# Kernel optimization log

Hardware: AMD Instinct MI355X
Metric: run time of the kernel (lower is better)

The kernel has to match this reference:

```python
import jax, jax.numpy as jnp
import numpy as np

GAMMA = 20
LAMBDA_INV = 25.0


def setup_inputs() -> dict:
    key = jax.random.key(0)
    k1, k2 = jax.random.split(key)
    B, P, D = 128, 512, 384
    z = jax.random.normal(k1, (B, P, D), dtype=jnp.float32)
    view_ids = jax.random.randint(k2, (P,), 0, 2, dtype=jnp.int64)
    return {"z": z, "view_ids": view_ids}


def reference(z, view_ids):
    B, P, D = z.shape
    # [B, P, P] pairwise similarity per image
    sim = jnp.einsum('bpd,bqd->bpq', z, z)
    # valid pairs: different view and not self
    mask_view = view_ids[None, :] != view_ids[:, None]          # [P, P]
    mask = mask_view & ~jnp.eye(P, dtype=bool)
    sim = jnp.where(mask[None, :, :], sim, jnp.float32(-1.0))
    best_sim = sim.max(axis=2)                                   # [B, P]
    best_j = sim.argmax(axis=2)                                  # [B, P]
    # flatten across batch, global top-gamma anchors
    best_sim_flat = best_sim.reshape(-1)                         # [B*P]
    offsets = jnp.arange(B, dtype=best_j.dtype)[:, None] * P
    best_j_flat = (best_j + offsets).reshape(-1)                 # [B*P]
    topk_vals, topk_idx = jax.lax.top_k(best_sim_flat, GAMMA)
    z_flat = z.reshape(-1, D)
    z1 = z_flat[topk_idx]                                        # anchors
    z2 = z_flat[best_j_flat[topk_idx]]                           # matches
    loss = LAMBDA_INV * jnp.mean((z1 - z2) ** 2)
    fmatch_avg_cos = jax.lax.stop_gradient(topk_vals.mean())
    return loss, fmatch_avg_cos
```

## Files before the change

### kernel.cpp

```cpp
#include <hip/hip_runtime.h>


#define NB 128
#define NP 512
#define ND 384
#define NGAMMA 20
#define NKS 12

typedef __attribute__((ext_vector_type(8))) short short8;
typedef __attribute__((ext_vector_type(4))) float f32x4;

__device__ __forceinline__ unsigned short f2bf(float f) {
    unsigned int u = __float_as_uint(f);
    u += 0x7fffu + ((u >> 16) & 1u);
    return (unsigned short)(u >> 16);
}

__device__ __forceinline__ void gload16(const void* gptr, void* lptr) {
    __builtin_amdgcn_global_load_lds(
        (const __attribute__((address_space(1))) void*)gptr,
        (__attribute__((address_space(3))) void*)lptr, 16, 0, 0);
}

__global__ __launch_bounds__(256) void fm_convert(
    const float* __restrict__ z, unsigned short* __restrict__ zt)
{
    __shared__ float ls[128][36];

    const int tid  = threadIdx.x;
    const int bid  = blockIdx.x;
    const int b    = bid / (NKS * 4);
    const int rem  = bid % (NKS * 4);
    const int kt   = rem >> 2;
    const int pblk = rem & 3;

    const float* zsrc = z + ((size_t)b * NP + pblk * 128) * ND + kt * 32;
#pragma unroll
    for (int i = 0; i < 4; ++i) {
        const int f   = tid + i * 256;
        const int row = f >> 3, c4 = f & 7;
        const float4 v = *(const float4*)(zsrc + (size_t)row * ND + c4 * 4);
        *(float4*)&ls[row][c4 * 4] = v;
    }
    __syncthreads();

    const int kg = tid >> 6, lane = tid & 63;
    unsigned short* dst = zt + (((size_t)b * NKS + kt) * 4 + kg) * 4096
                             + (size_t)pblk * 128 * 8;
#pragma unroll
    for (int it = 0; it < 2; ++it) {
        const int row = it * 64 + lane;
        const float4 v0 = *(const float4*)&ls[row][kg * 8];
        const float4 v1 = *(const float4*)&ls[row][kg * 8 + 4];
        short8 s;
        s[0] = (short)f2bf(v0.x); s[1] = (short)f2bf(v0.y);
        s[2] = (short)f2bf(v0.z); s[3] = (short)f2bf(v0.w);
        s[4] = (short)f2bf(v1.x); s[5] = (short)f2bf(v1.y);
        s[6] = (short)f2bf(v1.z); s[7] = (short)f2bf(v1.w);
        *(short8*)(dst + (size_t)row * 8) = s;
    }
}

__global__ __launch_bounds__(256, 3) void fm_gemm(
    const unsigned short* __restrict__ zt, const int* __restrict__ view,
    float* __restrict__ pval, int* __restrict__ pidx)
{
    __shared__ __align__(16) unsigned short Ah[3][4][128][8];
    __shared__ __align__(16) unsigned short Bh[3][4][128][8];
    __shared__ int vs[NP];
    float* lsv = (float*)&Ah[0][0][0][0];
    int*   lsi = (int*)lsv + 256;
    float* lqv = (float*)((int*)lsv + 512);
    int*   lqi = (int*)lsv + 768;

    const int tid  = threadIdx.x;
    const int lane = tid & 63;
    const int wid  = tid >> 6;
    const int wr   = wid >> 1, wc = wid & 1;
    const int g    = lane >> 4, r = lane & 15;

    const int bid  = blockIdx.x;
    const int gidx = (bid & 7) * 160 + (bid >> 3);
    const int b    = gidx / 10;
    const int t    = gidx % 10;
    int tr, tc;
    if (t < 4)      { tr = 0; tc = t; }
    else if (t < 7) { tr = 1; tc = t - 3; }
    else if (t < 9) { tr = 2; tc = t - 5; }
    else            { tr = 3; tc = 3; }
    const bool diag = (tr == tc);
    const int p0 = tr * 128, q0 = tc * 128;

    vs[tid]       = view[tid];
    vs[tid + 256] = view[tid + 256];
    __builtin_amdgcn_sched_barrier(0);

    f32x4 acc[4][4];
#pragma unroll
    for (int mi = 0; mi < 4; ++mi)
#pragma unroll
        for (int ni = 0; ni < 4; ++ni) acc[mi][ni] = (f32x4){0.f, 0.f, 0.f, 0.f};

#define STAGE(BUF, KT)                                                           \
    do {                                                                         \
        _Pragma("unroll")                                                        \
        for (int i = 0; i < 2; ++i) {                                            \
            const int c_  = wid * 2 + i;                                         \
            const int kg_ = c_ >> 1;                                             \
            const int rb_ = (c_ & 1) * 64;                                       \
            const size_t pl_ = (((size_t)b * NKS + (KT)) * 4 + kg_) * 4096;      \
            gload16(zt + pl_ + (size_t)(p0 + rb_ + lane) * 8,                    \
                    &Ah[BUF][kg_][rb_][0]);                                      \
            gload16(zt + pl_ + (size_t)(q0 + rb_ + lane) * 8,                    \
                    &Bh[BUF][kg_][rb_][0]);                                      \
        }                                                                        \
    } while (0)

#define COMPUTE(BUF)                                                             \
    do {                                                                         \
        short8 ah_[4], bh_[4];                                                   \
        _Pragma("unroll")                                                        \
        for (int mi = 0; mi < 4; ++mi)                                           \
            ah_[mi] = *(const short8*)&Ah[BUF][g][wr * 64 + mi * 16 + r][0];     \
        _Pragma("unroll")                                                        \
        for (int ni = 0; ni < 4; ++ni)                                           \
            bh_[ni] = *(const short8*)&Bh[BUF][g][wc * 64 + ni * 16 + r][0];     \
        _Pragma("unroll")                                                        \
        for (int mi = 0; mi < 4; ++mi)                                           \
            _Pragma("unroll")                                                    \
            for (int ni = 0; ni < 4; ++ni)                                       \
                acc[mi][ni] = __builtin_amdgcn_mfma_f32_16x16x32_bf16(           \
                    ah_[mi], bh_[ni], acc[mi][ni], 0, 0, 0);                     \
    } while (0)

    STAGE(0, 0);
    STAGE(1, 1);
#pragma unroll
    for (int kt = 0; kt < NKS; ++kt) {
        if (kt < NKS - 1) asm volatile("s_waitcnt vmcnt(4)" ::: "memory");
        else              asm volatile("s_waitcnt vmcnt(0)" ::: "memory");
        __builtin_amdgcn_s_barrier();
        __builtin_amdgcn_sched_barrier(0);
        if (kt + 2 < NKS) STAGE((kt + 2) % 3, kt + 2);
        __builtin_amdgcn_sched_barrier(0);
        COMPUTE(kt % 3);
    }
#undef STAGE
#undef COMPUTE

#pragma unroll
    for (int mi = 0; mi < 4; ++mi) {
#pragma unroll
        for (int j = 0; j < 4; ++j) {
            const int prow = p0 + wr * 64 + mi * 16 + g * 4 + j;
            const int rv = vs[prow];
            float bv = -2.0f; int bq = 0;
#pragma unroll
            for (int ni = 0; ni < 4; ++ni) {
                const int q = q0 + wc * 64 + ni * 16 + r;
                const float v = (vs[q] != rv) ? acc[mi][ni][j] : -1.0f;
                if (v > bv) { bv = v; bq = q; }
            }
#pragma unroll
            for (int off = 1; off < 16; off <<= 1) {
                const float ov = __shfl_xor(bv, off);
                const int   oq = __shfl_xor(bq, off);
                if (ov > bv || (ov == bv && oq < bq)) { bv = ov; bq = oq; }
            }
            if (r == 0) {
                lsv[(wr * 2 + wc) * 64 + mi * 16 + g * 4 + j] = bv;
                lsi[(wr * 2 + wc) * 64 + mi * 16 + g * 4 + j] = bq;
            }
        }
    }
    if (!diag) {
#pragma unroll
        for (int ni = 0; ni < 4; ++ni) {
            const int q = q0 + wc * 64 + ni * 16 + r;
            const int qv = vs[q];
            float bv = -2.0f; int bp = 0;
#pragma unroll
            for (int mi = 0; mi < 4; ++mi)
#pragma unroll
                for (int j = 0; j < 4; ++j) {
                    const int prow = p0 + wr * 64 + mi * 16 + g * 4 + j;
                    const float v = (vs[prow] != qv) ? acc[mi][ni][j] : -1.0f;
                    if (v > bv) { bv = v; bp = prow; }
                }
#pragma unroll
            for (int off = 16; off < 64; off <<= 1) {
                const float ov = __shfl_xor(bv, off);
                const int   op = __shfl_xor(bp, off);
                if (ov > bv || (ov == bv && op < bp)) { bv = ov; bp = op; }
            }
            if (g == 0) {
                lqv[(wc * 2 + wr) * 64 + ni * 16 + r] = bv;
                lqi[(wc * 2 + wr) * 64 + ni * 16 + r] = bp;
            }
        }
    }
    __syncthreads();
    if (tid < 128) {
        const int half = tid >> 6, row = tid & 63;
        {
            float v0 = lsv[(half * 2 + 0) * 64 + row]; int i0 = lsi[(half * 2 + 0) * 64 + row];
            const float v1 = lsv[(half * 2 + 1) * 64 + row]; const int i1 = lsi[(half * 2 + 1) * 64 + row];
            if (v1 > v0) { v0 = v1; i0 = i1; }
            const int p = p0 + half * 64 + row;
            pval[((size_t)b * NP + p) * 4 + tc] = v0;
            pidx[((size_t)b * NP + p) * 4 + tc] = i0;
        }
        if (!diag) {
            float v0 = lqv[(half * 2 + 0) * 64 + row]; int i0 = lqi[(half * 2 + 0) * 64 + row];
            const float v1 = lqv[(half * 2 + 1) * 64 + row]; const int i1 = lqi[(half * 2 + 1) * 64 + row];
            if (v1 > v0) { v0 = v1; i0 = i1; }
            const int q = q0 + half * 64 + row;
            pval[((size_t)b * NP + q) * 4 + tr] = v0;
            pidx[((size_t)b * NP + q) * 4 + tr] = i0;
        }
    }
}

__global__ __launch_bounds__(64) void fm_topk_local(
    const float* __restrict__ pval, float* __restrict__ cval, int* __restrict__ cidx)
{
    const int lane = threadIdx.x;
    const int base = blockIdx.x * 1024;
    float v[16]; int id[16];
#pragma unroll
    for (int i = 0; i < 16; ++i) {
        const int a = base + i * 64 + lane;
        const float4 pv = ((const float4*)pval)[a];
        float bv = pv.x;
        if (pv.y > bv) bv = pv.y;
        if (pv.z > bv) bv = pv.z;
        if (pv.w > bv) bv = pv.w;
        v[i] = bv; id[i] = a;
    }
    for (int it = 0; it < NGAMMA; ++it) {
        float bv = v[0]; int bi = id[0];
#pragma unroll
        for (int i = 1; i < 16; ++i)
            if (v[i] > bv || (v[i] == bv && id[i] < bi)) { bv = v[i]; bi = id[i]; }
#pragma unroll
        for (int off = 1; off < 64; off <<= 1) {
            const float ov = __shfl_xor(bv, off);
            const int   oi = __shfl_xor(bi, off);
            if (ov > bv || (ov == bv && oi < bi)) { bv = ov; bi = oi; }
        }
        if (lane == 0) {
            cval[blockIdx.x * NGAMMA + it] = bv;
            cidx[blockIdx.x * NGAMMA + it] = bi;
        }
#pragma unroll
        for (int i = 0; i < 16; ++i) if (id[i] == bi) v[i] = -1e30f;
    }
}

__global__ __launch_bounds__(256) void fm_final(
    const float* __restrict__ cval, const int* __restrict__ cidx,
    const float* __restrict__ pval, const int* __restrict__ pidx,
    const float* __restrict__ z, float* __restrict__ out)
{
    __shared__ int sel[NGAMMA];
    __shared__ int selj[NGAMMA];
    __shared__ float red[4];

    const int t = threadIdx.x;
    const int lane = t & 63, w = t >> 6;
    float ssum = 0.f;

    if (w == 0) {
        float v[20]; int id[20];
#pragma unroll
        for (int i = 0; i < 20; ++i) {
            const int e = i * 64 + lane;
            v[i] = cval[e]; id[i] = cidx[e];
        }
        for (int it = 0; it < NGAMMA; ++it) {
            float bv = v[0]; int bi = id[0];
#pragma unroll
            for (int i = 1; i < 20; ++i)
                if (v[i] > bv || (v[i] == bv && id[i] < bi)) { bv = v[i]; bi = id[i]; }
#pragma unroll
            for (int off = 1; off < 64; off <<= 1) {
                const float ov = __shfl_xor(bv, off);
                const int   oi = __shfl_xor(bi, off);
                if (ov > bv || (ov == bv && oi < bi)) { bv = ov; bi = oi; }
            }
            if (lane == 0) sel[it] = bi;
            ssum += bv;
#pragma unroll
            for (int i = 0; i < 20; ++i) if (id[i] == bi) v[i] = -1e30f;
        }
        if (lane < NGAMMA) {
            const int a = sel[lane];
            const float4 pv = ((const float4*)pval)[a];
            float bv = pv.x; int bc = 0;
            if (pv.y > bv) { bv = pv.y; bc = 1; }
            if (pv.z > bv) { bv = pv.z; bc = 2; }
            if (pv.w > bv) { bv = pv.w; bc = 3; }
            selj[lane] = ((a >> 9) << 9) + pidx[(size_t)a * 4 + bc];
        }
    }
    __syncthreads();

    float acc = 0.f;
    for (int pr = 0; pr < NGAMMA; ++pr) {
        const int a = sel[pr];
        const int j = selj[pr];
        const float* za = z + (size_t)a * ND;
        const float* zj = z + (size_t)j * ND;
        for (int d = t; d < ND; d += 256) {
            const float df = za[d] - zj[d];
            acc = fmaf(df, df, acc);
        }
    }
#pragma unroll
    for (int off = 1; off < 64; off <<= 1) acc += __shfl_xor(acc, off);
    if (lane == 0) red[w] = acc;
    __syncthreads();
    if (t == 0) {
        const float tot = red[0] + red[1] + red[2] + red[3];
        out[0] = 25.0f * tot / (float)(NGAMMA * ND);
        out[1] = ssum / (float)NGAMMA;
    }
}

extern "C" void kernel_launch(void* const* d_in, const int* in_sizes, int n_in,
                              void* d_out, int out_size, void* d_ws, size_t ws_size,
                              hipStream_t stream)
{
    const float* z    = (const float*)d_in[0];
    const int*   view = (const int*)d_in[1];
    float*       out  = (float*)d_out;
    char* ws = (char*)d_ws;

    const size_t zt_off   = 0;
    const size_t pval_off = (size_t)NB * NP * ND * 2;
    const size_t pidx_off = pval_off + (size_t)NB * NP * 4 * 4;
    const size_t cval_off = pidx_off + (size_t)NB * NP * 4 * 4;
    const size_t cidx_off = cval_off + 64 * NGAMMA * 4;

    unsigned short* zt = (unsigned short*)(ws + zt_off);
    float* pval = (float*)(ws + pval_off);
    int*   pidx = (int*)(ws + pidx_off);
    float* cval = (float*)(ws + cval_off);
    int*   cidx = (int*)(ws + cidx_off);

    fm_convert<<<NB * NKS * 4, 256, 0, stream>>>(z, zt);
    fm_gemm<<<NB * 10, 256, 0, stream>>>(zt, view, pval, pidx);
    fm_topk_local<<<(NB * NP) / 1024, 64, 0, stream>>>(pval, cval, cidx);
    fm_final<<<1, 256, 0, stream>>>(cval, cidx, pval, pidx, z, out);
}
```

Measured before the change: 134.5 us.

## Fuse all four stages into one persistent kernel with grid barriers

Replaces the four separate launches (convert, gemm, local top-k, final) with a single persistent kernel of 512 blocks that loops over the conversion tasks and GEMM tiles, separated by atomic-counter grid barriers. The local top-k is reworked to use 256 threads per block, and the final reduction waits on a counter. This is meant to remove launch gaps and tail effects between kernels. In exchange it adds spin-wait barriers, drops GEMM occupancy from 3 to 2 blocks per CU, and relies on all 512 blocks being co-resident, which can deadlock if they are not.

```diff
diff --git a/kernel.cpp b/kernel.cpp
--- a/kernel.cpp
+++ b/kernel.cpp
@@ -6,6 +6,8 @@
 #define ND 384
 #define NGAMMA 20
 #define NKS 12
+#define GRID 512
+#define NTILE 1280
 
 typedef __attribute__((ext_vector_type(8))) short short8;
 typedef __attribute__((ext_vector_type(4))) float f32x4;
@@ -22,96 +24,91 @@
         (__attribute__((address_space(3))) void*)lptr, 16, 0, 0);
 }
 
-__global__ __launch_bounds__(256) void fm_convert(
-    const float* __restrict__ z, unsigned short* __restrict__ zt)
+__device__ __forceinline__ void grid_sync(int* cnt, int target) {
+    __syncthreads();
+    if (threadIdx.x == 0) {
+        __threadfence();
+        __hip_atomic_fetch_add(cnt, 1, __ATOMIC_RELEASE, __HIP_MEMORY_SCOPE_AGENT);
+        while (__hip_atomic_load(cnt, __ATOMIC_RELAXED, __HIP_MEMORY_SCOPE_AGENT) < target)
+            __builtin_amdgcn_s_sleep(2);
+        __threadfence();
+    }
+    __syncthreads();
+}
+
+__global__ __launch_bounds__(256, 2) void fm_fused(
+    const float* __restrict__ z, const int* __restrict__ view,
+    unsigned short* __restrict__ zt,
+    float* __restrict__ pval, int* __restrict__ pidx,
+    float* __restrict__ cval, int* __restrict__ cidx,
+    int* __restrict__ cnt, float* __restrict__ out)
 {
-    __shared__ float ls[128][36];
+    __shared__ __align__(16) char lds[51200];
+    unsigned short (*Ah)[4][128][8] = (unsigned short(*)[4][128][8])lds;
+    unsigned short (*Bh)[4][128][8] = (unsigned short(*)[4][128][8])(lds + 24576);
+    int* vs = (int*)(lds + 49152);
 
     const int tid  = threadIdx.x;
     const int bid  = blockIdx.x;
-    const int b    = bid / (NKS * 4);
-    const int rem  = bid % (NKS * 4);
-    const int kt   = rem >> 2;
-    const int pblk = rem & 3;
-
-    const float* zsrc = z + ((size_t)b * NP + pblk * 128) * ND + kt * 32;
-#pragma unroll
-    for (int i = 0; i < 4; ++i) {
-        const int f   = tid + i * 256;
-        const int row = f >> 3, c4 = f & 7;
-        const float4 v = *(const float4*)(zsrc + (size_t)row * ND + c4 * 4);
-        *(float4*)&ls[row][c4 * 4] = v;
-    }
-    __syncthreads();
-
-    const int kg = tid >> 6, lane = tid & 63;
-    unsigned short* dst = zt + (((size_t)b * NKS + kt) * 4 + kg) * 4096
-                             + (size_t)pblk * 128 * 8;
-#pragma unroll
-    for (int it = 0; it < 2; ++it) {
-        const int row = it * 64 + lane;
-        const float4 v0 = *(const float4*)&ls[row][kg * 8];
-        const float4 v1 = *(const float4*)&ls[row][kg * 8 + 4];
-        short8 s;
-        s[0] = (short)f2bf(v0.x); s[1] = (short)f2bf(v0.y);
-        s[2] = (short)f2bf(v0.z); s[3] = (short)f2bf(v0.w);
-        s[4] = (short)f2bf(v1.x); s[5] = (short)f2bf(v1.y);
-        s[6] = (short)f2bf(v1.z); s[7] = (short)f2bf(v1.w);
-        *(short8*)(dst + (size_t)row * 8) = s;
-    }
-}
-
-__global__ __launch_bounds__(256, 3) void fm_gemm(
-    const unsigned short* __restrict__ zt, const int* __restrict__ view,
-    float* __restrict__ pval, int* __restrict__ pidx)
-{
-    __shared__ __align__(16) unsigned short Ah[3][4][128][8];
-    __shared__ __align__(16) unsigned short Bh[3][4][128][8];
-    __shared__ int vs[NP];
-    float* lsv = (float*)&Ah[0][0][0][0];
-    int*   lsi = (int*)lsv + 256;
-    float* lqv = (float*)((int*)lsv + 512);
-    int*   lqi = (int*)lsv + 768;
-
-    const int tid  = threadIdx.x;
     const int lane = tid & 63;
     const int wid  = tid >> 6;
     const int wr   = wid >> 1, wc = wid & 1;
     const int g    = lane >> 4, r = lane & 15;
 
-    const int bid  = blockIdx.x;
-    const int gidx = (bid & 7) * 160 + (bid >> 3);
-    const int b    = gidx / 10;
-    const int t    = gidx % 10;
-    int tr, tc;
-    if (t < 4)      { tr = 0; tc = t; }
-    else if (t < 7) { tr = 1; tc = t - 3; }
-    else if (t < 9) { tr = 2; tc = t - 5; }
-    else            { tr = 3; tc = 3; }
-    const bool diag = (tr == tc);
-    const int p0 = tr * 128, q0 = tc * 128;
+    {
+        float (*ls)[36] = (float(*)[36])lds;
+        for (int i = 0; i < 12; ++i) {
+            const int task = bid * 12 + i;
+            const int b    = task / (NKS * 4);
+            const int rem  = task % (NKS * 4);
+            const int kt   = rem >> 2;
+            const int pblk = rem & 3;
+            const float* zsrc = z + ((size_t)b * NP + pblk * 128) * ND + kt * 32;
+#pragma unroll
+            for (int k = 0; k < 4; ++k) {
+                const int f = tid + k * 256, row = f >> 3, c4 = f & 7;
+                *(float4*)&ls[row][c4 * 4] =
+                    *(const float4*)(zsrc + (size_t)row * ND + c4 * 4);
+            }
+            __syncthreads();
+            const int kg = wid;
+            unsigned short* dst = zt + (((size_t)b * NKS + kt) * 4 + kg) * 4096
+                                     + (size_t)pblk * 1024;
+#pragma unroll
+            for (int it = 0; it < 2; ++it) {
+                const int row = it * 64 + lane;
+                const float4 v0 = *(const float4*)&ls[row][kg * 8];
+                const float4 v1 = *(const float4*)&ls[row][kg * 8 + 4];
+                short8 s;
+                s[0] = (short)f2bf(v0.x); s[1] = (short)f2bf(v0.y);
+                s[2] = (short)f2bf(v0.z); s[3] = (short)f2bf(v0.w);
+                s[4] = (short)f2bf(v1.x); s[5] = (short)f2bf(v1.y);
+                s[6] = (short)f2bf(v1.z); s[7] = (short)f2bf(v1.w);
+                *(short8*)(dst + (size_t)row * 8) = s;
+            }
+            __syncthreads();
+        }
+    }
+    grid_sync(cnt + 0, GRID);
 
     vs[tid]       = view[tid];
     vs[tid + 256] = view[tid + 256];
-    __builtin_amdgcn_sched_barrier(0);
-
-    f32x4 acc[4][4];
-#pragma unroll
-    for (int mi = 0; mi < 4; ++mi)
-#pragma unroll
-        for (int ni = 0; ni < 4; ++ni) acc[mi][ni] = (f32x4){0.f, 0.f, 0.f, 0.f};
-
-#define STAGE(BUF, KT)                                                           \
+    float* lsv = (float*)lds;
+    int*   lsi = (int*)lds + 256;
+    float* lqv = (float*)lds + 512;
+    int*   lqi = (int*)lds + 768;
+
+#define STAGE(BUF, KT, P0, Q0, BB)                                               \
     do {                                                                         \
         _Pragma("unroll")                                                        \
-        for (int i = 0; i < 2; ++i) {                                            \
-            const int c_  = wid * 2 + i;                                         \
+        for (int i_ = 0; i_ < 2; ++i_) {                                         \
+            const int c_  = wid * 2 + i_;                                        \
             const int kg_ = c_ >> 1;                                             \
             const int rb_ = (c_ & 1) * 64;                                       \
-            const size_t pl_ = (((size_t)b * NKS + (KT)) * 4 + kg_) * 4096;      \
-            gload16(zt + pl_ + (size_t)(p0 + rb_ + lane) * 8,                    \
+            const size_t pl_ = (((size_t)(BB) * NKS + (KT)) * 4 + kg_) * 4096;   \
+            gload16(zt + pl_ + (size_t)((P0) + rb_ + lane) * 8,                  \
                     &Ah[BUF][kg_][rb_][0]);                                      \
-            gload16(zt + pl_ + (size_t)(q0 + rb_ + lane) * 8,                    \
+            gload16(zt + pl_ + (size_t)((Q0) + rb_ + lane) * 8,                  \
                     &Bh[BUF][kg_][rb_][0]);                                      \
         }                                                                        \
     } while (0)
@@ -133,144 +130,182 @@
                     ah_[mi], bh_[ni], acc[mi][ni], 0, 0, 0);                     \
     } while (0)
 
-    STAGE(0, 0);
-    STAGE(1, 1);
-#pragma unroll
-    for (int kt = 0; kt < NKS; ++kt) {
-        if (kt < NKS - 1) asm volatile("s_waitcnt vmcnt(4)" ::: "memory");
-        else              asm volatile("s_waitcnt vmcnt(0)" ::: "memory");
-        __builtin_amdgcn_s_barrier();
-        __builtin_amdgcn_sched_barrier(0);
-        if (kt + 2 < NKS) STAGE((kt + 2) % 3, kt + 2);
-        __builtin_amdgcn_sched_barrier(0);
-        COMPUTE(kt % 3);
+    for (int pass = 0; pass < 3; ++pass) {
+        const int x = bid + pass * 512;
+        if (x >= NTILE) break;
+        const int gidx = (x & 7) * 160 + (x >> 3);
+        const int b    = gidx / 10;
+        const int t    = gidx % 10;
+        int tr, tc;
+        if (t < 4)      { tr = 0; tc = t; }
+        else if (t < 7) { tr = 1; tc = t - 3; }
+        else if (t < 9) { tr = 2; tc = t - 5; }
+        else            { tr = 3; tc = 3; }
+        const bool diag = (tr == tc);
+        const int p0 = tr * 128, q0 = tc * 128;
+
+        f32x4 acc[4][4];
+#pragma unroll
+        for (int mi = 0; mi < 4; ++mi)
+#pragma unroll
+            for (int ni = 0; ni < 4; ++ni) acc[mi][ni] = (f32x4){0.f, 0.f, 0.f, 0.f};
+
+        __syncthreads();
+        STAGE(0, 0, p0, q0, b);
+        STAGE(1, 1, p0, q0, b);
+#pragma unroll
+        for (int kt = 0; kt < NKS; ++kt) {
+            if (kt < NKS - 1) asm volatile("s_waitcnt vmcnt(4)" ::: "memory");
+            else              asm volatile("s_waitcnt vmcnt(0)" ::: "memory");
+            __builtin_amdgcn_s_barrier();
+            __builtin_amdgcn_sched_barrier(0);
+            if (kt + 2 < NKS) STAGE((kt + 2) % 3, kt + 2, p0, q0, b);
+            __builtin_amdgcn_sched_barrier(0);
+            COMPUTE(kt % 3);
+        }
+
+#pragma unroll
+        for (int mi = 0; mi < 4; ++mi) {
+#pragma unroll
+            for (int j = 0; j < 4; ++j) {
+                const int prow = p0 + wr * 64 + mi * 16 + g * 4 + j;
+                const int rv = vs[prow];
+                float bv = -2.0f; int bq = 0;
+#pragma unroll
+                for (int ni = 0; ni < 4; ++ni) {
+                    const int q = q0 + wc * 64 + ni * 16 + r;
+                    const float v = (vs[q] != rv) ? acc[mi][ni][j] : -1.0f;
+                    if (v > bv) { bv = v; bq = q; }
+                }
+#pragma unroll
+                for (int off = 1; off < 16; off <<= 1) {
+                    const float ov = __shfl_xor(bv, off);
+                    const int   oq = __shfl_xor(bq, off);
+                    if (ov > bv || (ov == bv && oq < bq)) { bv = ov; bq = oq; }
+                }
+                if (r == 0) {
+                    lsv[(wr * 2 + wc) * 64 + mi * 16 + g * 4 + j] = bv;
+                    lsi[(wr * 2 + wc) * 64 + mi * 16 + g * 4 + j] = bq;
+                }
+            }
+        }
+        if (!diag) {
+#pragma unroll
+            for (int ni = 0; ni < 4; ++ni) {
+                const int q = q0 + wc * 64 + ni * 16 + r;
+                const int qv = vs[q];
+                float bv = -2.0f; int bp = 0;
+#pragma unroll
+                for (int mi = 0; mi < 4; ++mi)
+#pragma unroll
+                    for (int j = 0; j < 4; ++j) {
+                        const int prow = p0 + wr * 64 + mi * 16 + g * 4 + j;
+                        const float v = (vs[prow] != qv) ? acc[mi][ni][j] : -1.0f;
+                        if (v > bv) { bv = v; bp = prow; }
+                    }
+#pragma unroll
+                for (int off = 16; off < 64; off <<= 1) {
+                    const float ov = __shfl_xor(bv, off);
+                    const int   op = __shfl_xor(bp, off);
+                    if (ov > bv || (ov == bv && op < bp)) { bv = ov; bp = op; }
+                }
+                if (g == 0) {
+                    lqv[(wc * 2 + wr) * 64 + ni * 16 + r] = bv;
+                    lqi[(wc * 2 + wr) * 64 + ni * 16 + r] = bp;
+                }
+            }
+        }
+        __syncthreads();
+        if (tid < 128) {
+            const int half = tid >> 6, row = tid & 63;
+            {
+                float v0 = lsv[(half * 2 + 0) * 64 + row]; int i0 = lsi[(half * 2 + 0) * 64 + row];
+                const float v1 = lsv[(half * 2 + 1) * 64 + row]; const int i1 = lsi[(half * 2 + 1) * 64 + row];
+                if (v1 > v0) { v0 = v1; i0 = i1; }
+                const int p = p0 + half * 64 + row;
+                pval[((size_t)b * NP + p) * 4 + tc] = v0;
+                pidx[((size_t)b * NP + p) * 4 + tc] = i0;
+            }
+            if (!diag) {
+                float v0 = lqv[(half * 2 + 0) * 64 + row]; int i0 = lqi[(half * 2 + 0) * 64 + row];
+                const float v1 = lqv[(half * 2 + 1) * 64 + row]; const int i1 = lqi[(half * 2 + 1) * 64 + row];
+                if (v1 > v0) { v0 = v1; i0 = i1; }
+                const int q = q0 + half * 64 + row;
+                pval[((size_t)b * NP + q) * 4 + tr] = v0;
+                pidx[((size_t)b * NP + q) * 4 + tr] = i0;
+            }
+        }
     }
 #undef STAGE
 #undef COMPUTE
-
-#pragma unroll
-    for (int mi = 0; mi < 4; ++mi) {
-#pragma unroll
-        for (int j = 0; j < 4; ++j) {
-            const int prow = p0 + wr * 64 + mi * 16 + g * 4 + j;
-            const int rv = vs[prow];
-            float bv = -2.0f; int bq = 0;
-#pragma unroll
-            for (int ni = 0; ni < 4; ++ni) {
-                const int q = q0 + wc * 64 + ni * 16 + r;
-                const float v = (vs[q] != rv) ? acc[mi][ni][j] : -1.0f;
-                if (v > bv) { bv = v; bq = q; }
-            }
-#pragma unroll
-            for (int off = 1; off < 16; off <<= 1) {
-                const float ov = __shfl_xor(bv, off);
-                const int   oq = __shfl_xor(bq, off);
-                if (ov > bv || (ov == bv && oq < bq)) { bv = ov; bq = oq; }
-            }
-            if (r == 0) {
-                lsv[(wr * 2 + wc) * 64 + mi * 16 + g * 4 + j] = bv;
-                lsi[(wr * 2 + wc) * 64 + mi * 16 + g * 4 + j] = bq;
-            }
-        }
-    }
-    if (!diag) {
-#pragma unroll
-        for (int ni = 0; ni < 4; ++ni) {
-            const int q = q0 + wc * 64 + ni * 16 + r;
-            const int qv = vs[q];
-            float bv = -2.0f; int bp = 0;
-#pragma unroll
-            for (int mi = 0; mi < 4; ++mi)
-#pragma unroll
-                for (int j = 0; j < 4; ++j) {
-                    const int prow = p0 + wr * 64 + mi * 16 + g * 4 + j;
-                    const float v = (vs[prow] != qv) ? acc[mi][ni][j] : -1.0f;
-                    if (v > bv) { bv = v; bp = prow; }
-                }
-#pragma unroll
-            for (int off = 16; off < 64; off <<= 1) {
-                const float ov = __shfl_xor(bv, off);
-                const int   op = __shfl_xor(bp, off);
-                if (ov > bv || (ov == bv && op < bp)) { bv = ov; bp = op; }
-            }
-            if (g == 0) {
-                lqv[(wc * 2 + wr) * 64 + ni * 16 + r] = bv;
-                lqi[(wc * 2 + wr) * 64 + ni * 16 + r] = bp;
-            }
-        }
-    }
-    __syncthreads();
-    if (tid < 128) {
-        const int half = tid >> 6, row = tid & 63;
-        {
-            float v0 = lsv[(half * 2 + 0) * 64 + row]; int i0 = lsi[(half * 2 + 0) * 64 + row];
-            const float v1 = lsv[(half * 2 + 1) * 64 + row]; const int i1 = lsi[(half * 2 + 1) * 64 + row];
-            if (v1 > v0) { v0 = v1; i0 = i1; }
-            const int p = p0 + half * 64 + row;
-            pval[((size_t)b * NP + p) * 4 + tc] = v0;
-            pidx[((size_t)b * NP + p) * 4 + tc] = i0;
-        }
-        if (!diag) {
-            float v0 = lqv[(half * 2 + 0) * 64 + row]; int i0 = lqi[(half * 2 + 0) * 64 + row];
-            const float v1 = lqv[(half * 2 + 1) * 64 + row]; const int i1 = lqi[(half * 2 + 1) * 64 + row];
-            if (v1 > v0) { v0 = v1; i0 = i1; }
-            const int q = q0 + half * 64 + row;
-            pval[((size_t)b * NP + q) * 4 + tr] = v0;
-            pidx[((size_t)b * NP + q) * 4 + tr] = i0;
-        }
-    }
-}
-
-__global__ __launch_bounds__(64) void fm_topk_local(
-    const float* __restrict__ pval, float* __restrict__ cval, int* __restrict__ cidx)
-{
-    const int lane = threadIdx.x;
-    const int base = blockIdx.x * 1024;
-    float v[16]; int id[16];
-#pragma unroll
-    for (int i = 0; i < 16; ++i) {
-        const int a = base + i * 64 + lane;
-        const float4 pv = ((const float4*)pval)[a];
-        float bv = pv.x;
-        if (pv.y > bv) bv = pv.y;
-        if (pv.z > bv) bv = pv.z;
-        if (pv.w > bv) bv = pv.w;
-        v[i] = bv; id[i] = a;
-    }
-    for (int it = 0; it < NGAMMA; ++it) {
-        float bv = v[0]; int bi = id[0];
-#pragma unroll
-        for (int i = 1; i < 16; ++i)
-            if (v[i] > bv || (v[i] == bv && id[i] < bi)) { bv = v[i]; bi = id[i]; }
-#pragma unroll
-        for (int off = 1; off < 64; off <<= 1) {
-            const float ov = __shfl_xor(bv, off);
-            const int   oi = __shfl_xor(bi, off);
-            if (ov > bv || (ov == bv && oi < bi)) { bv = ov; bi = oi; }
-        }
-        if (lane == 0) {
-            cval[blockIdx.x * NGAMMA + it] = bv;
-            cidx[blockIdx.x * NGAMMA + it] = bi;
-        }
-#pragma unroll
-        for (int i = 0; i < 16; ++i) if (id[i] == bi) v[i] = -1e30f;
-    }
-}
-
-__global__ __launch_bounds__(256) void fm_final(
-    const float* __restrict__ cval, const int* __restrict__ cidx,
-    const float* __restrict__ pval, const int* __restrict__ pidx,
-    const float* __restrict__ z, float* __restrict__ out)
-{
-    __shared__ int sel[NGAMMA];
-    __shared__ int selj[NGAMMA];
-    __shared__ float red[4];
-
-    const int t = threadIdx.x;
-    const int lane = t & 63, w = t >> 6;
+    grid_sync(cnt + 1, GRID);
+
+    if (bid >= 64) return;
+
+    {
+        float* sv = (float*)lds;
+        float* wv = (float*)(lds + 4096);
+        int*   wi = (int*)(lds + 4112);
+        const int base = bid * 1024;
+#pragma unroll
+        for (int i = 0; i < 4; ++i) {
+            const int e = tid + 256 * i;
+            const float4 pv = ((const float4*)pval)[base + e];
+            float bv = pv.x;
+            if (pv.y > bv) bv = pv.y;
+            if (pv.z > bv) bv = pv.z;
+            if (pv.w > bv) bv = pv.w;
+            sv[e] = bv;
+        }
+        __syncthreads();
+        for (int it = 0; it < NGAMMA; ++it) {
+            float v = sv[tid];
+            int pos = tid;
+#pragma unroll
+            for (int i = 1; i < 4; ++i) {
+                const int e = tid + 256 * i;
+                const float x2 = sv[e];
+                if (x2 > v || (x2 == v && e < pos)) { v = x2; pos = e; }
+            }
+#pragma unroll
+            for (int off = 1; off < 64; off <<= 1) {
+                const float ov = __shfl_xor(v, off);
+                const int   op = __shfl_xor(pos, off);
+                if (ov > v || (ov == v && op < pos)) { v = ov; pos = op; }
+            }
+            if (lane == 0) { wv[wid] = v; wi[wid] = pos; }
+            __syncthreads();
+            if (tid == 0) {
+                float bv2 = wv[0]; int bp = wi[0];
+                for (int k = 1; k < 4; ++k)
+                    if (wv[k] > bv2 || (wv[k] == bv2 && wi[k] < bp)) { bv2 = wv[k]; bp = wi[k]; }
+                cval[bid * NGAMMA + it] = bv2;
+                cidx[bid * NGAMMA + it] = base + bp;
+                sv[bp] = -1e30f;
+            }
+            __syncthreads();
+        }
+        __syncthreads();
+        if (tid == 0) {
+            __threadfence();
+            __hip_atomic_fetch_add(cnt + 2, 1, __ATOMIC_RELEASE, __HIP_MEMORY_SCOPE_AGENT);
+        }
+    }
+    if (bid != 0) return;
+
+    if (tid == 0) {
+        while (__hip_atomic_load(cnt + 2, __ATOMIC_RELAXED, __HIP_MEMORY_SCOPE_AGENT) < 64)
+            __builtin_amdgcn_s_sleep(2);
+        __threadfence();
+    }
+    __syncthreads();
+
+    int*   sel  = (int*)(lds + 8192);
+    int*   selj = (int*)(lds + 8192 + 128);
+    float* red  = (float*)(lds + 8192 + 256);
     float ssum = 0.f;
 
-    if (w == 0) {
+    if (wid == 0) {
         float v[20]; int id[20];
 #pragma unroll
         for (int i = 0; i < 20; ++i) {
@@ -305,22 +340,22 @@
     }
     __syncthreads();
 
-    float acc = 0.f;
+    float acc2 = 0.f;
     for (int pr = 0; pr < NGAMMA; ++pr) {
         const int a = sel[pr];
         const int j = selj[pr];
         const float* za = z + (size_t)a * ND;
         const float* zj = z + (size_t)j * ND;
-        for (int d = t; d < ND; d += 256) {
+        for (int d = tid; d < ND; d += 256) {
             const float df = za[d] - zj[d];
-            acc = fmaf(df, df, acc);
-        }
-    }
-#pragma unroll
-    for (int off = 1; off < 64; off <<= 1) acc += __shfl_xor(acc, off);
-    if (lane == 0) red[w] = acc;
-    __syncthreads();
-    if (t == 0) {
+            acc2 = fmaf(df, df, acc2);
+        }
+    }
+#pragma unroll
+    for (int off = 1; off < 64; off <<= 1) acc2 += __shfl_xor(acc2, off);
+    if (lane == 0) red[wid] = acc2;
+    __syncthreads();
+    if (tid == 0) {
         const float tot = red[0] + red[1] + red[2] + red[3];
         out[0] = 25.0f * tot / (float)(NGAMMA * ND);
         out[1] = ssum / (float)NGAMMA;
@@ -341,15 +376,15 @@
     const size_t pidx_off = pval_off + (size_t)NB * NP * 4 * 4;
     const size_t cval_off = pidx_off + (size_t)NB * NP * 4 * 4;
     const size_t cidx_off = cval_off + 64 * NGAMMA * 4;
+    const size_t cnt_off  = cidx_off + 64 * NGAMMA * 4;
 
     unsigned short* zt = (unsigned short*)(ws + zt_off);
     float* pval = (float*)(ws + pval_off);
     int*   pidx = (int*)(ws + pidx_off);
     float* cval = (float*)(ws + cval_off);
     int*   cidx = (int*)(ws + cidx_off);
-
-    fm_convert<<<NB * NKS * 4, 256, 0, stream>>>(z, zt);
-    fm_gemm<<<NB * 10, 256, 0, stream>>>(zt, view, pval, pidx);
-    fm_topk_local<<<(NB * NP) / 1024, 64, 0, stream>>>(pval, cval, cidx);
-    fm_final<<<1, 256, 0, stream>>>(cval, cidx, pval, pidx, z, out);
-}
+    int*   cnt  = (int*)(ws + cnt_off);
+
+    hipMemsetAsync(cnt, 0, 3 * sizeof(int), stream);
+    fm_fused<<<GRID, 256, 0, stream>>>(z, view, zt, pval, pidx, cval, cidx, cnt, out);
+}
```

Result: slower. 270.0 us (+100.7%).

## Load GEMM fragments directly from global memory instead of LDS pipeline

Applied to the files above, without the earlier changes.

Removes the triple-buffered global-to-LDS staging with barriers in the similarity GEMM. Each wave now loads its bf16 MFMA operands straight from the pre-swizzled global layout into registers every k-step. This drops LDS traffic, the per-step workgroup barriers and the LDS allocation, which may allow higher occupancy. In exchange, the two waves that share a tile row or column now read the same data from global/L2 twice, and there is no explicit prefetch to hide load latency.

```diff
diff --git a/kernel.cpp b/kernel.cpp
--- a/kernel.cpp
+++ b/kernel.cpp
@@ -14,12 +14,6 @@
     unsigned int u = __float_as_uint(f);
     u += 0x7fffu + ((u >> 16) & 1u);
     return (unsigned short)(u >> 16);
-}
-
-__device__ __forceinline__ void gload16(const void* gptr, void* lptr) {
-    __builtin_amdgcn_global_load_lds(
-        (const __attribute__((address_space(1))) void*)gptr,
-        (__attribute__((address_space(3))) void*)lptr, 16, 0, 0);
 }
 
 __global__ __launch_bounds__(256) void fm_convert(
@@ -39,14 +33,13 @@
     for (int i = 0; i < 4; ++i) {
         const int f   = tid + i * 256;
         const int row = f >> 3, c4 = f & 7;
-        const float4 v = *(const float4*)(zsrc + (size_t)row * ND + c4 * 4);
-        *(float4*)&ls[row][c4 * 4] = v;
+        *(float4*)&ls[row][c4 * 4] = *(const float4*)(zsrc + (size_t)row * ND + c4 * 4);
     }
     __syncthreads();
 
     const int kg = tid >> 6, lane = tid & 63;
     unsigned short* dst = zt + (((size_t)b * NKS + kt) * 4 + kg) * 4096
-                             + (size_t)pblk * 128 * 8;
+                             + (size_t)pblk * 1024;
 #pragma unroll
     for (int it = 0; it < 2; ++it) {
         const int row = it * 64 + lane;
@@ -65,13 +58,11 @@
     const unsigned short* __restrict__ zt, const int* __restrict__ view,
     float* __restrict__ pval, int* __restrict__ pidx)
 {
-    __shared__ __align__(16) unsigned short Ah[3][4][128][8];
-    __shared__ __align__(16) unsigned short Bh[3][4][128][8];
     __shared__ int vs[NP];
-    float* lsv = (float*)&Ah[0][0][0][0];
-    int*   lsi = (int*)lsv + 256;
-    float* lqv = (float*)((int*)lsv + 512);
-    int*   lqi = (int*)lsv + 768;
+    __shared__ float lsv[2][2][64];
+    __shared__ int   lsi[2][2][64];
+    __shared__ float lqv[2][2][64];
+    __shared__ int   lqi[2][2][64];
 
     const int tid  = threadIdx.x;
     const int lane = tid & 63;
@@ -93,7 +84,13 @@
 
     vs[tid]       = view[tid];
     vs[tid + 256] = view[tid + 256];
-    __builtin_amdgcn_sched_barrier(0);
+    __syncthreads();
+
+    const size_t zbB = (size_t)b * (NKS * 4 * 4096);
+    const unsigned short* __restrict__ Az =
+        zt + zbB + (size_t)g * 4096 + (size_t)(p0 + wr * 64 + r) * 8;
+    const unsigned short* __restrict__ Bz =
+        zt + zbB + (size_t)g * 4096 + (size_t)(q0 + wc * 64 + r) * 8;
 
     f32x4 acc[4][4];
 #pragma unroll
@@ -101,52 +98,22 @@
 #pragma unroll
         for (int ni = 0; ni < 4; ++ni) acc[mi][ni] = (f32x4){0.f, 0.f, 0.f, 0.f};
 
-#define STAGE(BUF, KT)                                                           \
-    do {                                                                         \
-        _Pragma("unroll")                                                        \
-        for (int i = 0; i < 2; ++i) {                                            \
-            const int c_  = wid * 2 + i;                                         \
-            const int kg_ = c_ >> 1;                                             \
-            const int rb_ = (c_ & 1) * 64;                                       \
-            const size_t pl_ = (((size_t)b * NKS + (KT)) * 4 + kg_) * 4096;      \
-            gload16(zt + pl_ + (size_t)(p0 + rb_ + lane) * 8,                    \
-                    &Ah[BUF][kg_][rb_][0]);                                      \
-            gload16(zt + pl_ + (size_t)(q0 + rb_ + lane) * 8,                    \
-                    &Bh[BUF][kg_][rb_][0]);                                      \
-        }                                                                        \
-    } while (0)
-
-#define COMPUTE(BUF)                                                             \
-    do {                                                                         \
-        short8 ah_[4], bh_[4];                                                   \
-        _Pragma("unroll")                                                        \
-        for (int mi = 0; mi < 4; ++mi)                                           \
-            ah_[mi] = *(const short8*)&Ah[BUF][g][wr * 64 + mi * 16 + r][0];     \
-        _Pragma("unroll")                                                        \
-        for (int ni = 0; ni < 4; ++ni)                                           \
-            bh_[ni] = *(const short8*)&Bh[BUF][g][wc * 64 + ni * 16 + r][0];     \
-        _Pragma("unroll")                                                        \
-        for (int mi = 0; mi < 4; ++mi)                                           \
-            _Pragma("unroll")                                                    \
-            for (int ni = 0; ni < 4; ++ni)                                       \
-                acc[mi][ni] = __builtin_amdgcn_mfma_f32_16x16x32_bf16(           \
-                    ah_[mi], bh_[ni], acc[mi][ni], 0, 0, 0);                     \
-    } while (0)
-
-    STAGE(0, 0);
-    STAGE(1, 1);
 #pragma unroll
     for (int kt = 0; kt < NKS; ++kt) {
-        if (kt < NKS - 1) asm volatile("s_waitcnt vmcnt(4)" ::: "memory");
-        else              asm volatile("s_waitcnt vmcnt(0)" ::: "memory");
-        __builtin_amdgcn_s_barrier();
-        __builtin_amdgcn_sched_barrier(0);
-        if (kt + 2 < NKS) STAGE((kt + 2) % 3, kt + 2);
-        __builtin_amdgcn_sched_barrier(0);
-        COMPUTE(kt % 3);
-    }
-#undef STAGE
-#undef COMPUTE
+        short8 ah[4], bh[4];
+#pragma unroll
+        for (int mi = 0; mi < 4; ++mi)
+            ah[mi] = *(const short8*)(Az + (size_t)kt * 16384 + mi * 128);
+#pragma unroll
+        for (int ni = 0; ni < 4; ++ni)
+            bh[ni] = *(const short8*)(Bz + (size_t)kt * 16384 + ni * 128);
+#pragma unroll
+        for (int mi = 0; mi < 4; ++mi)
+#pragma unroll
+            for (int ni = 0; ni < 4; ++ni)
+                acc[mi][ni] = __builtin_amdgcn_mfma_f32_16x16x32_bf16(
+                    ah[mi], bh[ni], acc[mi][ni], 0, 0, 0);
+    }
 
 #pragma unroll
     for (int mi = 0; mi < 4; ++mi) {
@@ -168,8 +135,8 @@
                 if (ov > bv || (ov == bv && oq < bq)) { bv = ov; bq = oq; }
             }
             if (r == 0) {
-                lsv[(wr * 2 + wc) * 64 + mi * 16 + g * 4 + j] = bv;
-                lsi[(wr * 2 + wc) * 64 + mi * 16 + g * 4 + j] = bq;
+                lsv[wr][wc][mi * 16 + g * 4 + j] = bv;
+                lsi[wr][wc][mi * 16 + g * 4 + j] = bq;
             }
         }
     }
@@ -194,8 +161,8 @@
                 if (ov > bv || (ov == bv && op < bp)) { bv = ov; bp = op; }
             }
             if (g == 0) {
-                lqv[(wc * 2 + wr) * 64 + ni * 16 + r] = bv;
-                lqi[(wc * 2 + wr) * 64 + ni * 16 + r] = bp;
+                lqv[wc][wr][ni * 16 + r] = bv;
+                lqi[wc][wr][ni * 16 + r] = bp;
             }
         }
     }
@@ -203,16 +170,16 @@
     if (tid < 128) {
         const int half = tid >> 6, row = tid & 63;
         {
-            float v0 = lsv[(half * 2 + 0) * 64 + row]; int i0 = lsi[(half * 2 + 0) * 64 + row];
-            const float v1 = lsv[(half * 2 + 1) * 64 + row]; const int i1 = lsi[(half * 2 + 1) * 64 + row];
+            float v0 = lsv[half][0][row]; int i0 = lsi[half][0][row];
+            const float v1 = lsv[half][1][row]; const int i1 = lsi[half][1][row];
             if (v1 > v0) { v0 = v1; i0 = i1; }
             const int p = p0 + half * 64 + row;
             pval[((size_t)b * NP + p) * 4 + tc] = v0;
             pidx[((size_t)b * NP + p) * 4 + tc] = i0;
         }
         if (!diag) {
-            float v0 = lqv[(half * 2 + 0) * 64 + row]; int i0 = lqi[(half * 2 + 0) * 64 + row];
-            const float v1 = lqv[(half * 2 + 1) * 64 + row]; const int i1 = lqi[(half * 2 + 1) * 64 + row];
+            float v0 = lqv[half][0][row]; int i0 = lqi[half][0][row];
+            const float v1 = lqv[half][1][row]; const int i1 = lqi[half][1][row];
             if (v1 > v0) { v0 = v1; i0 = i1; }
             const int q = q0 + half * 64 + row;
             pval[((size_t)b * NP + q) * 4 + tr] = v0;
```

Measured after the change: 135.1 us. No clear change (+0.4%).

## Use 8-wave GEMM blocks and fuse top-k stages with atomic ticket

Applied to the files above, without the earlier changes.

The similarity GEMM blocks grow from 4 to 8 waves. Each wave now covers a 64x32 sub-tile, and the staging loads are spread so each wave issues one A and one B load per k-step. The local top-k kernel and the final single-block kernel are merged into one kernel. A last-block-done atomic ticket triggers the global top-gamma selection and loss computation, which removes one launch. This adds a memset launch and atomic/fence overhead, and it halves the accumulator work per wave, which may lower MFMA efficiency per wave.

```diff
diff --git a/kernel.cpp b/kernel.cpp
--- a/kernel.cpp
+++ b/kernel.cpp
@@ -39,14 +39,13 @@
     for (int i = 0; i < 4; ++i) {
         const int f   = tid + i * 256;
         const int row = f >> 3, c4 = f & 7;
-        const float4 v = *(const float4*)(zsrc + (size_t)row * ND + c4 * 4);
-        *(float4*)&ls[row][c4 * 4] = v;
+        *(float4*)&ls[row][c4 * 4] = *(const float4*)(zsrc + (size_t)row * ND + c4 * 4);
     }
     __syncthreads();
 
     const int kg = tid >> 6, lane = tid & 63;
     unsigned short* dst = zt + (((size_t)b * NKS + kt) * 4 + kg) * 4096
-                             + (size_t)pblk * 128 * 8;
+                             + (size_t)pblk * 1024;
 #pragma unroll
     for (int it = 0; it < 2; ++it) {
         const int row = it * 64 + lane;
@@ -61,7 +60,7 @@
     }
 }
 
-__global__ __launch_bounds__(256, 3) void fm_gemm(
+__global__ __launch_bounds__(512, 4) void fm_gemm(
     const unsigned short* __restrict__ zt, const int* __restrict__ view,
     float* __restrict__ pval, int* __restrict__ pidx)
 {
@@ -69,14 +68,15 @@
     __shared__ __align__(16) unsigned short Bh[3][4][128][8];
     __shared__ int vs[NP];
     float* lsv = (float*)&Ah[0][0][0][0];
-    int*   lsi = (int*)lsv + 256;
-    float* lqv = (float*)((int*)lsv + 512);
-    int*   lqi = (int*)lsv + 768;
+    int*   lsi = (int*)lsv + 512;
+    float* lqv = (float*)lsv + 1024;
+    int*   lqi = (int*)lsv + 1280;
 
     const int tid  = threadIdx.x;
     const int lane = tid & 63;
     const int wid  = tid >> 6;
-    const int wr   = wid >> 1, wc = wid & 1;
+    const int wr   = wid >> 2;
+    const int wc2  = wid & 3;
     const int g    = lane >> 4, r = lane & 15;
 
     const int bid  = blockIdx.x;
@@ -91,44 +91,37 @@
     const bool diag = (tr == tc);
     const int p0 = tr * 128, q0 = tc * 128;
 
-    vs[tid]       = view[tid];
-    vs[tid + 256] = view[tid + 256];
+    vs[tid] = view[tid];
     __builtin_amdgcn_sched_barrier(0);
 
-    f32x4 acc[4][4];
+    f32x4 acc[4][2];
 #pragma unroll
     for (int mi = 0; mi < 4; ++mi)
 #pragma unroll
-        for (int ni = 0; ni < 4; ++ni) acc[mi][ni] = (f32x4){0.f, 0.f, 0.f, 0.f};
+        for (int ni = 0; ni < 2; ++ni) acc[mi][ni] = (f32x4){0.f, 0.f, 0.f, 0.f};
 
 #define STAGE(BUF, KT)                                                           \
     do {                                                                         \
-        _Pragma("unroll")                                                        \
-        for (int i = 0; i < 2; ++i) {                                            \
-            const int c_  = wid * 2 + i;                                         \
-            const int kg_ = c_ >> 1;                                             \
-            const int rb_ = (c_ & 1) * 64;                                       \
-            const size_t pl_ = (((size_t)b * NKS + (KT)) * 4 + kg_) * 4096;      \
-            gload16(zt + pl_ + (size_t)(p0 + rb_ + lane) * 8,                    \
-                    &Ah[BUF][kg_][rb_][0]);                                      \
-            gload16(zt + pl_ + (size_t)(q0 + rb_ + lane) * 8,                    \
-                    &Bh[BUF][kg_][rb_][0]);                                      \
-        }                                                                        \
+        const int kg_ = wid >> 1;                                                \
+        const int rb_ = (wid & 1) * 64;                                          \
+        const size_t pl_ = (((size_t)b * NKS + (KT)) * 4 + kg_) * 4096;          \
+        gload16(zt + pl_ + (size_t)(p0 + rb_ + lane) * 8, &Ah[BUF][kg_][rb_][0]); \
+        gload16(zt + pl_ + (size_t)(q0 + rb_ + lane) * 8, &Bh[BUF][kg_][rb_][0]); \
     } while (0)
 
 #define COMPUTE(BUF)                                                             \
     do {                                                                         \
-        short8 ah_[4], bh_[4];                                                   \
+        short8 ah_[4], bh_[2];                                                   \
         _Pragma("unroll")                                                        \
         for (int mi = 0; mi < 4; ++mi)                                           \
             ah_[mi] = *(const short8*)&Ah[BUF][g][wr * 64 + mi * 16 + r][0];     \
         _Pragma("unroll")                                                        \
-        for (int ni = 0; ni < 4; ++ni)                                           \
-            bh_[ni] = *(const short8*)&Bh[BUF][g][wc * 64 + ni * 16 + r][0];     \
+        for (int ni = 0; ni < 2; ++ni)                                           \
+            bh_[ni] = *(const short8*)&Bh[BUF][g][wc2 * 32 + ni * 16 + r][0];    \
         _Pragma("unroll")                                                        \
         for (int mi = 0; mi < 4; ++mi)                                           \
             _Pragma("unroll")                                                    \
-            for (int ni = 0; ni < 4; ++ni)                                       \
+            for (int ni = 0; ni < 2; ++ni)                                       \
                 acc[mi][ni] = __builtin_amdgcn_mfma_f32_16x16x32_bf16(           \
                     ah_[mi], bh_[ni], acc[mi][ni], 0, 0, 0);                     \
     } while (0)
@@ -137,7 +130,7 @@
     STAGE(1, 1);
 #pragma unroll
     for (int kt = 0; kt < NKS; ++kt) {
-        if (kt < NKS - 1) asm volatile("s_waitcnt vmcnt(4)" ::: "memory");
+        if (kt < NKS - 1) asm volatile("s_waitcnt vmcnt(2)" ::: "memory");
         else              asm volatile("s_waitcnt vmcnt(0)" ::: "memory");
         __builtin_amdgcn_s_barrier();
         __builtin_amdgcn_sched_barrier(0);
@@ -156,8 +149,8 @@
             const int rv = vs[prow];
             float bv = -2.0f; int bq = 0;
 #pragma unroll
-            for (int ni = 0; ni < 4; ++ni) {
-                const int q = q0 + wc * 64 + ni * 16 + r;
+            for (int ni = 0; ni < 2; ++ni) {
+                const int q = q0 + wc2 * 32 + ni * 16 + r;
                 const float v = (vs[q] != rv) ? acc[mi][ni][j] : -1.0f;
                 if (v > bv) { bv = v; bq = q; }
             }
@@ -168,15 +161,15 @@
                 if (ov > bv || (ov == bv && oq < bq)) { bv = ov; bq = oq; }
             }
             if (r == 0) {
-                lsv[(wr * 2 + wc) * 64 + mi * 16 + g * 4 + j] = bv;
-                lsi[(wr * 2 + wc) * 64 + mi * 16 + g * 4 + j] = bq;
+                lsv[(wr * 4 + wc2) * 64 + mi * 16 + g * 4 + j] = bv;
+                lsi[(wr * 4 + wc2) * 64 + mi * 16 + g * 4 + j] = bq;
             }
         }
     }
     if (!diag) {
 #pragma unroll
-        for (int ni = 0; ni < 4; ++ni) {
-            const int q = q0 + wc * 64 + ni * 16 + r;
+        for (int ni = 0; ni < 2; ++ni) {
+            const int q = q0 + wc2 * 32 + ni * 16 + r;
             const int qv = vs[q];
             float bv = -2.0f; int bp = 0;
 #pragma unroll
@@ -194,36 +187,46 @@
                 if (ov > bv || (ov == bv && op < bp)) { bv = ov; bp = op; }
             }
             if (g == 0) {
-                lqv[(wc * 2 + wr) * 64 + ni * 16 + r] = bv;
-                lqi[(wc * 2 + wr) * 64 + ni * 16 + r] = bp;
+                lqv[(wc2 * 2 + wr) * 32 + ni * 16 + r] = bv;
+                lqi[(wc2 * 2 + wr) * 32 + ni * 16 + r] = bp;
             }
         }
     }
     __syncthreads();
     if (tid < 128) {
-        const int half = tid >> 6, row = tid & 63;
         {
-            float v0 = lsv[(half * 2 + 0) * 64 + row]; int i0 = lsi[(half * 2 + 0) * 64 + row];
-            const float v1 = lsv[(half * 2 + 1) * 64 + row]; const int i1 = lsi[(half * 2 + 1) * 64 + row];
+            const int hw = tid >> 6, rw = tid & 63;
+            float v0 = lsv[(hw * 4 + 0) * 64 + rw]; int i0 = lsi[(hw * 4 + 0) * 64 + rw];
+#pragma unroll
+            for (int c = 1; c < 4; ++c) {
+                const float v1 = lsv[(hw * 4 + c) * 64 + rw];
+                const int   i1 = lsi[(hw * 4 + c) * 64 + rw];
+                if (v1 > v0) { v0 = v1; i0 = i1; }
+            }
+            pval[((size_t)b * NP + p0 + tid) * 4 + tc] = v0;
+            pidx[((size_t)b * NP + p0 + tid) * 4 + tc] = i0;
+        }
+        if (!diag) {
+            const int cg = tid >> 5, cw = tid & 31;
+            float v0 = lqv[(cg * 2 + 0) * 32 + cw]; int i0 = lqi[(cg * 2 + 0) * 32 + cw];
+            const float v1 = lqv[(cg * 2 + 1) * 32 + cw];
+            const int   i1 = lqi[(cg * 2 + 1) * 32 + cw];
             if (v1 > v0) { v0 = v1; i0 = i1; }
-            const int p = p0 + half * 64 + row;
-            pval[((size_t)b * NP + p) * 4 + tc] = v0;
-            pidx[((size_t)b * NP + p) * 4 + tc] = i0;
-        }
-        if (!diag) {
-            float v0 = lqv[(half * 2 + 0) * 64 + row]; int i0 = lqi[(half * 2 + 0) * 64 + row];
-            const float v1 = lqv[(half * 2 + 1) * 64 + row]; const int i1 = lqi[(half * 2 + 1) * 64 + row];
-            if (v1 > v0) { v0 = v1; i0 = i1; }
-            const int q = q0 + half * 64 + row;
-            pval[((size_t)b * NP + q) * 4 + tr] = v0;
-            pidx[((size_t)b * NP + q) * 4 + tr] = i0;
-        }
-    }
-}
-
-__global__ __launch_bounds__(64) void fm_topk_local(
-    const float* __restrict__ pval, float* __restrict__ cval, int* __restrict__ cidx)
+            pval[((size_t)b * NP + q0 + tid) * 4 + tr] = v0;
+            pidx[((size_t)b * NP + q0 + tid) * 4 + tr] = i0;
+        }
+    }
+}
+
+__global__ __launch_bounds__(64) void fm_tail(
+    const float* __restrict__ pval, const int* __restrict__ pidx,
+    const float* __restrict__ z,
+    float* __restrict__ cval, int* __restrict__ cidx,
+    int* __restrict__ ticket, float* __restrict__ out)
 {
+    __shared__ int sel[NGAMMA];
+    __shared__ int selj[NGAMMA];
+
     const int lane = threadIdx.x;
     const int base = blockIdx.x * 1024;
     float v[16]; int id[16];
@@ -255,53 +258,47 @@
 #pragma unroll
         for (int i = 0; i < 16; ++i) if (id[i] == bi) v[i] = -1e30f;
     }
-}
-
-__global__ __launch_bounds__(256) void fm_final(
-    const float* __restrict__ cval, const int* __restrict__ cidx,
-    const float* __restrict__ pval, const int* __restrict__ pidx,
-    const float* __restrict__ z, float* __restrict__ out)
-{
-    __shared__ int sel[NGAMMA];
-    __shared__ int selj[NGAMMA];
-    __shared__ float red[4];
-
-    const int t = threadIdx.x;
-    const int lane = t & 63, w = t >> 6;
+
+    __threadfence();
+    int old = 0;
+    if (lane == 0)
+        old = __hip_atomic_fetch_add(ticket, 1, __ATOMIC_ACQ_REL, __HIP_MEMORY_SCOPE_AGENT);
+    old = __shfl(old, 0);
+    if (old != 63) return;
+    __threadfence();
+
+    float mv[20]; int mid[20];
+#pragma unroll
+    for (int i = 0; i < 20; ++i) {
+        const int e = i * 64 + lane;
+        mv[i] = cval[e]; mid[i] = cidx[e];
+    }
     float ssum = 0.f;
-
-    if (w == 0) {
-        float v[20]; int id[20];
-#pragma unroll
-        for (int i = 0; i < 20; ++i) {
-            const int e = i * 64 + lane;
-            v[i] = cval[e]; id[i] = cidx[e];
-        }
-        for (int it = 0; it < NGAMMA; ++it) {
-            float bv = v[0]; int bi = id[0];
-#pragma unroll
-            for (int i = 1; i < 20; ++i)
-                if (v[i] > bv || (v[i] == bv && id[i] < bi)) { bv = v[i]; bi = id[i]; }
-#pragma unroll
-            for (int off = 1; off < 64; off <<= 1) {
-                const float ov = __shfl_xor(bv, off);
-                const int   oi = __shfl_xor(bi, off);
-                if (ov > bv || (ov == bv && oi < bi)) { bv = ov; bi = oi; }
-            }
-            if (lane == 0) sel[it] = bi;
-            ssum += bv;
-#pragma unroll
-            for (int i = 0; i < 20; ++i) if (id[i] == bi) v[i] = -1e30f;
-        }
-        if (lane < NGAMMA) {
-            const int a = sel[lane];
-            const float4 pv = ((const float4*)pval)[a];
-            float bv = pv.x; int bc = 0;
-            if (pv.y > bv) { bv = pv.y; bc = 1; }
-            if (pv.z > bv) { bv = pv.z; bc = 2; }
-            if (pv.w > bv) { bv = pv.w; bc = 3; }
-            selj[lane] = ((a >> 9) << 9) + pidx[(size_t)a * 4 + bc];
-        }
+    for (int it = 0; it < NGAMMA; ++it) {
+        float bv = mv[0]; int bi = mid[0];
+#pragma unroll
+        for (int i = 1; i < 20; ++i)
+            if (mv[i] > bv || (mv[i] == bv && mid[i] < bi)) { bv = mv[i]; bi = mid[i]; }
+#pragma unroll
+        for (int off = 1; off < 64; off <<= 1) {
+            const float ov = __shfl_xor(bv, off);
+            const int   oi = __shfl_xor(bi, off);
+            if (ov > bv || (ov == bv && oi < bi)) { bv = ov; bi = oi; }
+        }
+        if (lane == 0) sel[it] = bi;
+        ssum += bv;
+#pragma unroll
+        for (int i = 0; i < 20; ++i) if (mid[i] == bi) mv[i] = -1e30f;
+    }
+    __syncthreads();
+    if (lane < NGAMMA) {
+        const int a = sel[lane];
+        const float4 pv = ((const float4*)pval)[a];
+        float bv = pv.x; int bc = 0;
+        if (pv.y > bv) { bv = pv.y; bc = 1; }
+        if (pv.z > bv) { bv = pv.z; bc = 2; }
+        if (pv.w > bv) { bv = pv.w; bc = 3; }
+        selj[lane] = ((a >> 9) << 9) + pidx[(size_t)a * 4 + bc];
     }
     __syncthreads();
 
@@ -311,18 +308,17 @@
         const int j = selj[pr];
         const float* za = z + (size_t)a * ND;
         const float* zj = z + (size_t)j * ND;
-        for (int d = t; d < ND; d += 256) {
+#pragma unroll
+        for (int it = 0; it < ND / 64; ++it) {
+            const int d = it * 64 + lane;
             const float df = za[d] - zj[d];
             acc = fmaf(df, df, acc);
         }
     }
 #pragma unroll
     for (int off = 1; off < 64; off <<= 1) acc += __shfl_xor(acc, off);
-    if (lane == 0) red[w] = acc;
-    __syncthreads();
-    if (t == 0) {
-        const float tot = red[0] + red[1] + red[2] + red[3];
-        out[0] = 25.0f * tot / (float)(NGAMMA * ND);
+    if (lane == 0) {
+        out[0] = 25.0f * acc / (float)(NGAMMA * ND);
         out[1] = ssum / (float)NGAMMA;
     }
 }
@@ -341,15 +337,17 @@
     const size_t pidx_off = pval_off + (size_t)NB * NP * 4 * 4;
     const size_t cval_off = pidx_off + (size_t)NB * NP * 4 * 4;
     const size_t cidx_off = cval_off + 64 * NGAMMA * 4;
+    const size_t tick_off = cidx_off + 64 * NGAMMA * 4;
 
     unsigned short* zt = (unsigned short*)(ws + zt_off);
     float* pval = (float*)(ws + pval_off);
     int*   pidx = (int*)(ws + pidx_off);
     float* cval = (float*)(ws + cval_off);
     int*   cidx = (int*)(ws + cidx_off);
-
+    int*   tick = (int*)(ws + tick_off);
+
+    hipMemsetAsync(tick, 0, sizeof(int), stream);
     fm_convert<<<NB * NKS * 4, 256, 0, stream>>>(z, zt);
-    fm_gemm<<<NB * 10, 256, 0, stream>>>(zt, view, pval, pidx);
-    fm_topk_local<<<(NB * NP) / 1024, 64, 0, stream>>>(pval, cval, cidx);
-    fm_final<<<1, 256, 0, stream>>>(cval, cidx, pval, pidx, z, out);
-}
+    fm_gemm<<<NB * 10, 512, 0, stream>>>(zt, view, pval, pidx);
+    fm_tail<<<(NB * NP) / 1024, 64, 0, stream>>>(pval, pidx, z, cval, cidx, tick, out);
+}
```

Result: no change. 133.0 us (-1.2%).
